# Optimization experiments

Measured on AMD Instinct MI355X. Metric: run time of the kernel, lower is better.

The kernel has to match this reference:

```python
import jax, jax.numpy as jnp
import numpy as np

T, B, I, H = 256, 32, 128, 256
CLIP = 2.0

def setup_inputs() -> dict:
    key = jax.random.key(0)
    ks = jax.random.split(key, 10)
    si, sh = 1.0 / np.sqrt(I), 1.0 / np.sqrt(H)
    return {
        "x":     jax.random.normal(ks[0], (T, B, I), jnp.float32),
        "Wx":    jax.random.normal(ks[1], (4 * H, I), jnp.float32) * si,
        "bx":    jax.random.normal(ks[2], (4 * H,), jnp.float32) * si,
        "Wh":    jax.random.normal(ks[3], (4 * H, H), jnp.float32) * sh,
        "bh":    jax.random.normal(ks[4], (4 * H,), jnp.float32) * sh,
        "w_mod": jax.random.normal(ks[5], (1, H), jnp.float32) * sh,
        "b_mod": jax.random.normal(ks[6], (1,), jnp.float32) * sh,
        "w_fan": jax.random.normal(ks[7], (H, 1), jnp.float32),
        "b_fan": jax.random.normal(ks[8], (H,), jnp.float32),
        "alpha": 1e-4 * jax.random.uniform(ks[9], (H, H), jnp.float32),
    }

def reference(x, Wx, bx, Wh, bh, w_mod, b_mod, w_fan, b_fan, alpha):
    Bn = x.shape[1]
    # precompute input projection for all timesteps: [T, B, 4H]
    xf = jnp.einsum('tbi,gi->tbg', x, Wx) + bx

    def step(state, xf_t):
        h, c, hebb = state  # h,c: [B,H]; hebb: [B,H,H]
        fioj = xf_t + h @ Wh.T + bh                     # [B,4H]
        f = jax.nn.sigmoid(fioj[:, :H])
        i = jax.nn.sigmoid(fioj[:, H:2 * H])
        o = jax.nn.sigmoid(fioj[:, 2 * H:3 * H])
        # h_pred @ (alpha * hebb) : batched vec-mat product
        plast = jnp.einsum('bh,hk,bhk->bk', h, alpha, hebb)
        j = jnp.tanh(fioj[:, 3 * H:] + plast)
        c_new = f * c + i * j
        h_new = o * jnp.tanh(c_new)
        eta = jnp.tanh(c_new @ w_mod.T + b_mod)          # [B,1]
        myeta = eta * w_fan[:, 0] + b_fan                # [B,H] (Linear(1,H) fanout)
        # delta_hebb = outer(h_pred, j); eta modulates along the j axis
        hebb_new = jnp.clip(hebb + myeta[:, None, :] * (h[:, :, None] * j[:, None, :]),
                            -CLIP, CLIP)
        return (h_new, c_new, hebb_new), h_new

    init = (jnp.zeros((Bn, H), jnp.float32),
            jnp.zeros((Bn, H), jnp.float32),
            jnp.zeros((Bn, H, H), jnp.float32))
    (h, c, hebb), hs = jax.lax.scan(step, init, xf)
    return hs, h, c, hebb
```

## Files before the change

### kernel.cpp

```cpp
#include <hip/hip_runtime.h>


#define TT 256
#define BB 32
#define II 128
#define HH 256
#define G4 1024

typedef _Float16 h2_t __attribute__((ext_vector_type(2)));
typedef unsigned long long u64;

__device__ __forceinline__ float sigm(float x) {
    return 1.0f / (1.0f + __expf(-x));
}
__device__ __forceinline__ float tanhfast(float x) {
    return 1.0f - 2.0f / (__expf(2.0f * x) + 1.0f);
}
__device__ __forceinline__ unsigned pkh(float lo, float hi) {
    h2_t v;
    v.x = (_Float16)lo;
    v.y = (_Float16)hi;
    return __builtin_bit_cast(unsigned, v);
}

__device__ __forceinline__ void bar_lds() {
    asm volatile("s_waitcnt lgkmcnt(0)\n\ts_barrier" ::: "memory");
}

#if __has_builtin(__builtin_amdgcn_fdot2)
__device__ __forceinline__ float dot2(unsigned a, unsigned b, float c) {
    return __builtin_amdgcn_fdot2(__builtin_bit_cast(h2_t, a),
                                  __builtin_bit_cast(h2_t, b), c, false);
}
#else
__device__ __forceinline__ float dot2(unsigned a, unsigned b, float c) {
    h2_t av = __builtin_bit_cast(h2_t, a), bv = __builtin_bit_cast(h2_t, b);
    return c + (float)av.x * (float)bv.x + (float)av.y * (float)bv.y;
}
#endif

__device__ __forceinline__ h2_t pkfma(h2_t a, h2_t b, h2_t c) {
#if __has_builtin(__builtin_elementwise_fma)
    return __builtin_elementwise_fma(a, b, c);
#else
    return a * b + c;
#endif
}
__device__ __forceinline__ h2_t clip2h(h2_t x) {
    const h2_t lo = {(_Float16)-2.0f, (_Float16)-2.0f};
    const h2_t hi = {(_Float16)2.0f, (_Float16)2.0f};
#if __has_builtin(__builtin_elementwise_max) && __has_builtin(__builtin_elementwise_min)
    return __builtin_elementwise_min(__builtin_elementwise_max(x, lo), hi);
#else
    h2_t r = x;
    r.x = r.x < lo.x ? lo.x : (r.x > hi.x ? hi.x : r.x);
    r.y = r.y < lo.y ? lo.y : (r.y > hi.y ? hi.y : r.y);
    return r;
#endif
}

__device__ __forceinline__ void ld3_fast(const u64* p1, const u64* p2,
                                         const u64* p3,
                                         u64& v1, u64& v2, u64& v3) {
    asm volatile(
        "global_load_dwordx2 %0, %3, off sc0\n\t"
        "global_load_dwordx2 %1, %4, off sc0\n\t"
        "global_load_dwordx2 %2, %5, off sc0\n\t"
        "s_waitcnt vmcnt(0)"
        : "=&v"(v1), "=&v"(v2), "=&v"(v3)
        : "v"(p1), "v"(p2), "v"(p3));
}

__global__ __launch_bounds__(256) void prep_wd3(const float* __restrict__ Wh,
                                                uint4* __restrict__ Wd3) {
    int idx = blockIdx.x * 256 + threadIdx.x;
    int ro = idx >> 12, rem = idx & 4095;
    int g = rem >> 2, ri = rem & 3;
    int r8 = 4 * ro + ri;
    const float4* s = (const float4*)(Wh + (size_t)g * HH + (r8 << 3));
    float4 a = s[0], b2 = s[1];
    uint4 o;
    o.x = pkh(a.x, a.y);
    o.y = pkh(a.z, a.w);
    o.z = pkh(b2.x, b2.y);
    o.w = pkh(b2.z, b2.w);
    Wd3[idx] = o;
}

__global__ __launch_bounds__(256) void prep_alq(const float* __restrict__ alpha,
                                                uint4* __restrict__ alQ) {
    int idx = blockIdx.x * 256 + threadIdx.x;
    int p4 = idx >> 8, k = idx & 255;
    unsigned r[4];
#pragma unroll
    for (int j = 0; j < 4; ++j) {
        int p = 4 * p4 + j;
        float a0 = alpha[(size_t)(2 * p) * HH + k];
        float a1 = alpha[(size_t)(2 * p + 1) * HH + k];
        r[j] = pkh(a0, a1);
    }
    uint4 o; o.x = r[0]; o.y = r[1]; o.z = r[2]; o.w = r[3];
    alQ[idx] = o;
}

__global__ __launch_bounds__(256) void xf_gemm(const float* __restrict__ x,
                                               const float* __restrict__ Wx,
                                               const float* __restrict__ bx,
                                               const float* __restrict__ bh,
                                               float* __restrict__ xf) {
    __shared__ float As[64][37];
    __shared__ float Bs[64][37];
    const int tid = threadIdx.x;
    const int tx = tid & 15, ty = tid >> 4;
    const int m0 = blockIdx.y << 6;
    const int n0 = blockIdx.x << 6;
    float c[4][4] = {};

    for (int k0 = 0; k0 < II; k0 += 32) {
#pragma unroll
        for (int hh = 0; hh < 2; ++hh) {
            int row = (tid >> 3) + (hh << 5);
            int col = (tid & 7) << 2;
            float4 va = *(const float4*)(x + (size_t)(m0 + row) * II + k0 + col);
            As[row][col] = va.x; As[row][col + 1] = va.y;
            As[row][col + 2] = va.z; As[row][col + 3] = va.w;
            float4 vb = *(const float4*)(Wx + (size_t)(n0 + row) * II + k0 + col);
            Bs[row][col] = vb.x; Bs[row][col + 1] = vb.y;
            Bs[row][col + 2] = vb.z; Bs[row][col + 3] = vb.w;
        }
        __syncthreads();
#pragma unroll
        for (int kk = 0; kk < 32; ++kk) {
            float a[4], bb[4];
#pragma unroll
            for (int u = 0; u < 4; ++u) a[u] = As[(ty << 2) + u][kk];
#pragma unroll
            for (int v = 0; v < 4; ++v) bb[v] = Bs[(tx << 2) + v][kk];
#pragma unroll
            for (int u = 0; u < 4; ++u)
#pragma unroll
                for (int v = 0; v < 4; ++v)
                    c[u][v] = fmaf(a[u], bb[v], c[u][v]);
        }
        __syncthreads();
    }
    const int n = n0 + (tx << 2);
    float4 bxv = *(const float4*)(bx + n);
    float4 bhv = *(const float4*)(bh + n);
    float4 badd = {bxv.x + bhv.x, bxv.y + bhv.y, bxv.z + bhv.z, bxv.w + bhv.w};
#pragma unroll
    for (int u = 0; u < 4; ++u) {
        int m = m0 + (ty << 2) + u;
        float4 o = {c[u][0] + badd.x, c[u][1] + badd.y,
                    c[u][2] + badd.z, c[u][3] + badd.w};
        *(float4*)(xf + (size_t)m * G4 + n) = o;
    }
}

#define HBQ_FOREACH(X) X(0) X(1) X(2) X(3) X(4) X(5) X(6) X(7)

#define HBQ_DECL(i) h2_t hp##i = {(_Float16)0.0f, (_Float16)0.0f};
#define HBQ_OUT(i) \
    hbout[(size_t)(r0g + 2 * i) * HH + k]     = (float)hp##i.x; \
    hbout[(size_t)(r0g + 2 * i + 1) * HH + k] = (float)hp##i.y;

#define HBQ_STEP(i, au, hou, hnu) { \
    h2_t al2 = __builtin_bit_cast(h2_t, au); \
    h2_t ho2 = __builtin_bit_cast(h2_t, hou); \
    h2_t hn2 = __builtin_bit_cast(h2_t, hnu); \
    hp##i = clip2h(pkfma(mj2, ho2, hp##i)); \
    h2_t hna = hn2 * al2; \
    pp = dot2(__builtin_bit_cast(unsigned, hna), \
              __builtin_bit_cast(unsigned, hp##i), pp); }

#define HBQ_CHUNK(q, AV, i0, i1, i2, i3) { \
    uint4 ho = hfO4[hb4 + (q)]; \
    uint4 hn = hfN4[hb4 + (q)]; \
    HBQ_STEP(i0, AV.x, ho.x, hn.x) \
    HBQ_STEP(i1, AV.y, ho.y, hn.y) \
    HBQ_STEP(i2, AV.z, ho.z, hn.z) \
    HBQ_STEP(i3, AV.w, ho.w, hn.w) }

#define HBV_STEP(i, hou) { \
    h2_t ho2 = __builtin_bit_cast(h2_t, hou); \
    hp##i = clip2h(pkfma(mj2, ho2, hp##i)); }
#define HBV_CHUNK(q, i0, i1, i2, i3) { \
    uint4 ho = hfO4[hb4 + (q)]; \
    HBV_STEP(i0, ho.x) HBV_STEP(i1, ho.y) \
    HBV_STEP(i2, ho.z) HBV_STEP(i3, ho.w) }

#define DOTW(W, HV) { \
    ac0 = dot2(W.x, HV.x, ac0); ac1 = dot2(W.y, HV.y, ac1); \
    ac2 = dot2(W.z, HV.z, ac2); ac3 = dot2(W.w, HV.w, ac3); }

#define PUBLISH(val) { \
    u64 pkv = ((u64)tag << 32) | (u64)__builtin_bit_cast(unsigned, val); \
    __hip_atomic_store(&myF[off], pkv, __ATOMIC_RELAXED, \
                       __HIP_MEMORY_SCOPE_WORKGROUP); \
    __hip_atomic_store(&myEx[off], pkv, __ATOMIC_RELAXED, \
                       __HIP_MEMORY_SCOPE_AGENT); }

__global__ __launch_bounds__(1024, 1) void scan_kernel(
    const float* __restrict__ xf,
    const uint4* __restrict__ Wd3,
    const uint4* __restrict__ alQ,
    const float* __restrict__ w_mod,
    const float* __restrict__ b_mod,
    const float* __restrict__ w_fan,
    const float* __restrict__ b_fan,
    u64* __restrict__ exData,
    u64* __restrict__ exFast,
    float* __restrict__ out) {
    const int bid = blockIdx.x;
    const int r   = bid >> 5;
    const int b   = bid & 31;
    const int tid = threadIdx.x;
    const int k   = tid & (HH - 1);
    const int rg  = tid >> 8;
    const int r0g = r * 64 + rg * 16;
    const int hb4 = r0g >> 3;

    __shared__ alignas(16) unsigned short hf_s[2][HH];
    __shared__ float fioj_s[G4];
    __shared__ float pp_s[4][HH];
    __shared__ float red_s[4];

    HBQ_FOREACH(HBQ_DECL)

    if (tid < HH) {
        hf_s[0][tid] = 0;
        hf_s[1][tid] = 0;
    }
    if (tid < 4) red_s[tid] = 0.0f;
    __syncthreads();

    const float bmod = b_mod[0];
    const float wf = w_fan[k], bf = b_fan[k], wm = w_mod[k];
    float creg = 0.0f, jreg = 0.0f, hnreg = 0.0f;

    const uint4* wb = Wd3 + ((size_t)(2 * r) << 12) + (tid << 2);
    uint4 w0 = wb[0], w1 = wb[1], w2 = wb[2], w3 = wb[3];
    uint4 w4 = wb[4096], w5 = wb[4097], w6 = wb[4098], w7 = wb[4099];
    uint4 aqA = alQ[(size_t)(8 * r + 2 * rg) * 256 + k];
    uint4 aqB = alQ[(size_t)(8 * r + 2 * rg + 1) * 256 + k];

    const float* xfp = xf + (size_t)b * G4 + tid;
    float xcur = (rg == r) ? xfp[0] : 0.0f;

    u64* myEx = exData + (size_t)((b * 4 + r) * 2) * 1024;
    const u64* pEx1 = exData + (size_t)((b * 4 + ((r + 1) & 3)) * 2) * 1024;
    const u64* pEx2 = exData + (size_t)((b * 4 + ((r + 2) & 3)) * 2) * 1024;
    const u64* pEx3 = exData + (size_t)((b * 4 + ((r + 3) & 3)) * 2) * 1024;
    u64* myF = exFast + (size_t)((b * 4 + r) * 2) * 1024;
    const u64* pF1 = exFast + (size_t)((b * 4 + ((r + 1) & 3)) * 2) * 1024;
    const u64* pF2 = exFast + (size_t)((b * 4 + ((r + 2) & 3)) * 2) * 1024;
    const u64* pF3 = exFast + (size_t)((b * 4 + ((r + 3) & 3)) * 2) * 1024;

    for (int t = 0; t < TT; ++t) {
        float xnext = 0.0f;
        if (rg == r && t + 1 < TT) xnext = xfp[(size_t)(t + 1) * BB * G4];

        const unsigned tag = (unsigned)(t + 1);
        const int off = (t & 1) * 1024 + tid;

        float eta = tanhfast(((red_s[0] + red_s[1]) + (red_s[2] + red_s[3])) + bmod);
        float mj = fmaf(eta, wf, bf) * jreg;
        h2_t mj2;
        mj2.x = (_Float16)mj;
        mj2.y = mj2.x;
        const uint4* hfO4 = (const uint4*)hf_s[t & 1];
        const uint4* hfN4 = (const uint4*)hf_s[(t & 1) ^ 1];
        float pp = 0.0f;
        HBQ_CHUNK(0, aqA, 0, 1, 2, 3)
        HBQ_CHUNK(1, aqB, 4, 5, 6, 7)
        pp_s[rg][k] = pp;

        float ac0 = 0.f, ac1 = 0.f, ac2 = 0.f, ac3 = 0.f;
        {
            const int hx = r << 3;
            uint4 h0 = hfN4[hx], h1 = hfN4[hx + 1];
            uint4 h2 = hfN4[hx + 2], h3 = hfN4[hx + 3];
            DOTW(w0, h0) DOTW(w1, h1) DOTW(w2, h2) DOTW(w3, h3)
            uint4 h4 = hfN4[hx + 4], h5 = hfN4[hx + 5];
            uint4 h6 = hfN4[hx + 6], h7 = hfN4[hx + 7];
            DOTW(w4, h4) DOTW(w5, h5) DOTW(w6, h6) DOTW(w7, h7)
        }
        float part = ((ac0 + ac1) + (ac2 + ac3)) + xcur;
        xcur = xnext;

        if (tid < 768) PUBLISH(part)
        bar_lds();

        if (tid >= 768) {
            int k2 = tid - 768;
            part += (pp_s[0][k2] + pp_s[1][k2]) + (pp_s[2][k2] + pp_s[3][k2]);
            PUBLISH(part)
        }

        {
            float s1 = 0.f, s2 = 0.f, s3 = 0.f;
            bool d1 = false, d2 = false, d3 = false;
            const u64* f1 = pF1 + off;
            const u64* f2 = pF2 + off;
            const u64* f3 = pF3 + off;
            int it = 0;
            do {
                u64 v1, v2, v3;
                if ((it & 3) != 3) {
                    ld3_fast(f1, f2, f3, v1, v2, v3);
                } else {
                    v1 = __hip_atomic_load(pEx1 + off, __ATOMIC_RELAXED,
                                           __HIP_MEMORY_SCOPE_AGENT);
                    v2 = __hip_atomic_load(pEx2 + off, __ATOMIC_RELAXED,
                                           __HIP_MEMORY_SCOPE_AGENT);
                    v3 = __hip_atomic_load(pEx3 + off, __ATOMIC_RELAXED,
                                           __HIP_MEMORY_SCOPE_AGENT);
                }
                ++it;
                if (!d1 && (unsigned)(v1 >> 32) == tag) {
                    s1 = __builtin_bit_cast(float, (unsigned)v1);
                    d1 = true;
                }
                if (!d2 && (unsigned)(v2 >> 32) == tag) {
                    s2 = __builtin_bit_cast(float, (unsigned)v2);
                    d2 = true;
                }
                if (!d3 && (unsigned)(v3 >> 32) == tag) {
                    s3 = __builtin_bit_cast(float, (unsigned)v3);
                    d3 = true;
                }
            } while (!(d1 && d2 && d3));
            fioj_s[tid] = part + ((s1 + s2) + s3);
        }
        bar_lds();

        jreg = tanhfast(fioj_s[3 * HH + k]);
        if (rg == 0) {
            float fg = sigm(fioj_s[k]);
            float ig = sigm(fioj_s[HH + k]);
            float og = sigm(fioj_s[2 * HH + k]);
            creg = fmaf(fg, creg, ig * jreg);
            hnreg = og * tanhfast(creg);
            _Float16 hh = (_Float16)hnreg;
            hf_s[t & 1][k] = __builtin_bit_cast(unsigned short, hh);
            if (r == 0) out[((size_t)t * BB + b) * HH + k] = hnreg;
            float e = creg * wm;
#pragma unroll
            for (int m = 32; m >= 1; m >>= 1) e += __shfl_xor(e, m, 64);
            if ((k & 63) == 0) red_s[k >> 6] = e;
        }
        bar_lds();
    }

    {
        float eta = tanhfast(((red_s[0] + red_s[1]) + (red_s[2] + red_s[3])) + bmod);
        float mj = fmaf(eta, wf, bf) * jreg;
        h2_t mj2;
        mj2.x = (_Float16)mj;
        mj2.y = mj2.x;
        const uint4* hfO4 = (const uint4*)hf_s[0];
        HBV_CHUNK(0, 0, 1, 2, 3)
        HBV_CHUNK(1, 4, 5, 6, 7)
    }

    const size_t HS = (size_t)TT * BB * HH;
    if (r == 0 && rg == 0) {
        out[HS + (size_t)b * HH + k]           = hnreg;
        out[HS + BB * HH + (size_t)b * HH + k] = creg;
    }
    float* hbout = out + HS + 2 * BB * HH + (size_t)b * HH * HH;
    HBQ_FOREACH(HBQ_OUT)
}

extern "C" void kernel_launch(void* const* d_in, const int* in_sizes, int n_in,
                              void* d_out, int out_size, void* d_ws,
                              size_t ws_size, hipStream_t stream) {
    const float* x     = (const float*)d_in[0];
    const float* Wx    = (const float*)d_in[1];
    const float* bx    = (const float*)d_in[2];
    const float* Wh    = (const float*)d_in[3];
    const float* bh    = (const float*)d_in[4];
    const float* w_mod = (const float*)d_in[5];
    const float* b_mod = (const float*)d_in[6];
    const float* w_fan = (const float*)d_in[7];
    const float* b_fan = (const float*)d_in[8];
    const float* alpha = (const float*)d_in[9];
    float* out = (float*)d_out;

    float* xf  = (float*)d_ws;
    uint4* Wd3 = (uint4*)((char*)d_ws + 33554432);
    uint4* alQ = (uint4*)((char*)d_ws + 34078720);
    u64*   exD = (u64*)((char*)d_ws + 34209792);
    u64*   exF = (u64*)((char*)d_ws + 36306944);

    hipLaunchKernelGGL(prep_wd3, dim3(128), dim3(256), 0, stream, Wh, Wd3);
    hipLaunchKernelGGL(prep_alq, dim3(32), dim3(256), 0, stream, alpha, alQ);
    hipLaunchKernelGGL(xf_gemm, dim3(16, 128), dim3(256), 0, stream,
                       x, Wx, bx, bh, xf);
    hipLaunchKernelGGL(scan_kernel, dim3(128), dim3(1024), 0, stream,
                       xf, Wd3, alQ, w_mod, b_mod, w_fan, b_fan,
                       exD, exF, out);
}
```

Before: 758.7 us.

## Interleave gate rows so each thread quad computes LSTM cell via shuffles

The recurrent weight rows are permuted so the four gates of one hidden unit land in adjacent lanes of a thread quad. Each thread applies its gate activation in place and exchanges the four values through lane shuffles, and all 1024 threads run the cell update redundantly. This removes the fioj shared-memory round trip and one block barrier per timestep, and spreads the transcendental work across all threads. In exchange it adds shuffle and select overhead, redundant cell updates, and a 16-way reduction for eta.

```diff
diff --git a/kernel.cpp b/kernel.cpp
--- a/kernel.cpp
+++ b/kernel.cpp
@@ -75,10 +75,11 @@
                                                 uint4* __restrict__ Wd3) {
     int idx = blockIdx.x * 256 + threadIdx.x;
     int ro = idx >> 12, rem = idx & 4095;
-    int g = rem >> 2, ri = rem & 3;
+    int s = rem >> 2, ri = rem & 3;
+    int g = (s & 3) * 256 + (s >> 2);
     int r8 = 4 * ro + ri;
-    const float4* s = (const float4*)(Wh + (size_t)g * HH + (r8 << 3));
-    float4 a = s[0], b2 = s[1];
+    const float4* src = (const float4*)(Wh + (size_t)g * HH + (r8 << 3));
+    float4 a = src[0], b2 = src[1];
     uint4 o;
     o.x = pkh(a.x, a.y);
     o.y = pkh(a.z, a.w);
@@ -173,9 +174,9 @@
     pp = dot2(__builtin_bit_cast(unsigned, hna), \
               __builtin_bit_cast(unsigned, hp##i), pp); }
 
-#define HBQ_CHUNK(q, AV, i0, i1, i2, i3) { \
-    uint4 ho = hfO4[hb4 + (q)]; \
-    uint4 hn = hfN4[hb4 + (q)]; \
+#define HBQ_CHUNK(cq, AV, i0, i1, i2, i3) { \
+    uint4 ho = hfO4[hb4 + (cq)]; \
+    uint4 hn = hfN4[hb4 + (cq)]; \
     HBQ_STEP(i0, AV.x, ho.x, hn.x) \
     HBQ_STEP(i1, AV.y, ho.y, hn.y) \
     HBQ_STEP(i2, AV.z, ho.z, hn.z) \
@@ -184,8 +185,8 @@
 #define HBV_STEP(i, hou) { \
     h2_t ho2 = __builtin_bit_cast(h2_t, hou); \
     hp##i = clip2h(pkfma(mj2, ho2, hp##i)); }
-#define HBV_CHUNK(q, i0, i1, i2, i3) { \
-    uint4 ho = hfO4[hb4 + (q)]; \
+#define HBV_CHUNK(cq, i0, i1, i2, i3) { \
+    uint4 ho = hfO4[hb4 + (cq)]; \
     HBV_STEP(i0, ho.x) HBV_STEP(i1, ho.y) \
     HBV_STEP(i2, ho.z) HBV_STEP(i3, ho.w) }
 
@@ -199,6 +200,14 @@
                        __HIP_MEMORY_SCOPE_WORKGROUP); \
     __hip_atomic_store(&myEx[off], pkv, __ATOMIC_RELAXED, \
                        __HIP_MEMORY_SCOPE_AGENT); }
+
+#define ETA16() ({ \
+    const float4* rp_ = (const float4*)red_s; \
+    float4 e0_ = rp_[0], e1_ = rp_[1], e2_ = rp_[2], e3_ = rp_[3]; \
+    (((e0_.x + e0_.y) + (e0_.z + e0_.w)) + \
+     ((e1_.x + e1_.y) + (e1_.z + e1_.w))) + \
+    (((e2_.x + e2_.y) + (e2_.z + e2_.w)) + \
+     ((e3_.x + e3_.y) + (e3_.z + e3_.w))); })
 
 __global__ __launch_bounds__(1024, 1) void scan_kernel(
     const float* __restrict__ xf,
@@ -215,28 +224,35 @@
     const int r   = bid >> 5;
     const int b   = bid & 31;
     const int tid = threadIdx.x;
+    const int wv  = tid >> 6;
+    const int l   = tid & 63;
+    const int q   = tid & 3;
+    const int kc  = tid >> 2;
+    const int g   = (q << 8) + kc;
     const int k   = tid & (HH - 1);
     const int rg  = tid >> 8;
     const int r0g = r * 64 + rg * 16;
     const int hb4 = r0g >> 3;
 
     __shared__ alignas(16) unsigned short hf_s[2][HH];
-    __shared__ float fioj_s[G4];
     __shared__ float pp_s[4][HH];
-    __shared__ float red_s[4];
+    __shared__ float js_s[HH];
+    __shared__ alignas(16) float red_s[16];
 
     HBQ_FOREACH(HBQ_DECL)
 
     if (tid < HH) {
         hf_s[0][tid] = 0;
         hf_s[1][tid] = 0;
-    }
-    if (tid < 4) red_s[tid] = 0.0f;
+        js_s[tid] = 0.0f;
+    }
+    if (tid < 16) red_s[tid] = 0.0f;
     __syncthreads();
 
     const float bmod = b_mod[0];
-    const float wf = w_fan[k], bf = b_fan[k], wm = w_mod[k];
-    float creg = 0.0f, jreg = 0.0f, hnreg = 0.0f;
+    const float wf = w_fan[k], bf = b_fan[k];
+    const float wmq = 0.25f * w_mod[kc];
+    float creg = 0.0f, hreg = 0.0f;
 
     const uint4* wb = Wd3 + ((size_t)(2 * r) << 12) + (tid << 2);
     uint4 w0 = wb[0], w1 = wb[1], w2 = wb[2], w3 = wb[3];
@@ -244,8 +260,8 @@
     uint4 aqA = alQ[(size_t)(8 * r + 2 * rg) * 256 + k];
     uint4 aqB = alQ[(size_t)(8 * r + 2 * rg + 1) * 256 + k];
 
-    const float* xfp = xf + (size_t)b * G4 + tid;
-    float xcur = (rg == r) ? xfp[0] : 0.0f;
+    const float* xfp = xf + (size_t)b * G4 + g;
+    float xcur = (q == r) ? xfp[0] : 0.0f;
 
     u64* myEx = exData + (size_t)((b * 4 + r) * 2) * 1024;
     const u64* pEx1 = exData + (size_t)((b * 4 + ((r + 1) & 3)) * 2) * 1024;
@@ -258,13 +274,14 @@
 
     for (int t = 0; t < TT; ++t) {
         float xnext = 0.0f;
-        if (rg == r && t + 1 < TT) xnext = xfp[(size_t)(t + 1) * BB * G4];
+        if (q == r && t + 1 < TT) xnext = xfp[(size_t)(t + 1) * BB * G4];
 
         const unsigned tag = (unsigned)(t + 1);
         const int off = (t & 1) * 1024 + tid;
 
-        float eta = tanhfast(((red_s[0] + red_s[1]) + (red_s[2] + red_s[3])) + bmod);
-        float mj = fmaf(eta, wf, bf) * jreg;
+        float eta = tanhfast(ETA16() + bmod);
+        float jls = js_s[k];
+        float mj = fmaf(eta, wf, bf) * jls;
         h2_t mj2;
         mj2.x = (_Float16)mj;
         mj2.y = mj2.x;
@@ -288,15 +305,15 @@
         float part = ((ac0 + ac1) + (ac2 + ac3)) + xcur;
         xcur = xnext;
 
-        if (tid < 768) PUBLISH(part)
+        if (q != 3) PUBLISH(part)
         bar_lds();
 
-        if (tid >= 768) {
-            int k2 = tid - 768;
-            part += (pp_s[0][k2] + pp_s[1][k2]) + (pp_s[2][k2] + pp_s[3][k2]);
+        if (q == 3) {
+            part += (pp_s[0][kc] + pp_s[1][kc]) + (pp_s[2][kc] + pp_s[3][kc]);
             PUBLISH(part)
         }
 
+        float tot;
         {
             float s1 = 0.f, s2 = 0.f, s3 = 0.f;
             bool d1 = false, d2 = false, d3 = false;
@@ -330,31 +347,45 @@
                     d3 = true;
                 }
             } while (!(d1 && d2 && d3));
-            fioj_s[tid] = part + ((s1 + s2) + s3);
-        }
+            tot = part + ((s1 + s2) + s3);
+        }
+
+        float scale = (q == 3) ? 2.0f : 1.0f;
+        float sg = 1.0f / (1.0f + __expf(-scale * tot));
+        float act = fmaf(sg, scale, (q == 3) ? -1.0f : 0.0f);
+
+        float x1v = __shfl_xor(act, 1, 64);
+        float x2v = __shfl_xor(act, 2, 64);
+        float x3v = __shfl_xor(x1v, 2, 64);
+        bool sA = (q & 1) != 0, sB = (q & 2) != 0;
+        float b0 = sA ? x1v : act;
+        float b1 = sA ? act : x1v;
+        float b2v = sA ? x3v : x2v;
+        float b3v = sA ? x2v : x3v;
+        float fg = sB ? b2v : b0;
+        float og = sB ? b0 : b2v;
+        float ig = sB ? b3v : b1;
+        float jg = sB ? b1 : b3v;
+
+        creg = fmaf(fg, creg, ig * jg);
+        hreg = og * tanhfast(creg);
+        if (q == 0) {
+            _Float16 hh = (_Float16)hreg;
+            hf_s[t & 1][kc] = __builtin_bit_cast(unsigned short, hh);
+            js_s[kc] = jg;
+            if (r == 0) out[((size_t)t * BB + b) * HH + kc] = hreg;
+        }
+        float e = creg * wmq;
+#pragma unroll
+        for (int m = 32; m >= 1; m >>= 1) e += __shfl_xor(e, m, 64);
+        if (l == 0) red_s[wv] = e;
+
         bar_lds();
-
-        jreg = tanhfast(fioj_s[3 * HH + k]);
-        if (rg == 0) {
-            float fg = sigm(fioj_s[k]);
-            float ig = sigm(fioj_s[HH + k]);
-            float og = sigm(fioj_s[2 * HH + k]);
-            creg = fmaf(fg, creg, ig * jreg);
-            hnreg = og * tanhfast(creg);
-            _Float16 hh = (_Float16)hnreg;
-            hf_s[t & 1][k] = __builtin_bit_cast(unsigned short, hh);
-            if (r == 0) out[((size_t)t * BB + b) * HH + k] = hnreg;
-            float e = creg * wm;
-#pragma unroll
-            for (int m = 32; m >= 1; m >>= 1) e += __shfl_xor(e, m, 64);
-            if ((k & 63) == 0) red_s[k >> 6] = e;
-        }
-        bar_lds();
     }
 
     {
-        float eta = tanhfast(((red_s[0] + red_s[1]) + (red_s[2] + red_s[3])) + bmod);
-        float mj = fmaf(eta, wf, bf) * jreg;
+        float eta = tanhfast(ETA16() + bmod);
+        float mj = fmaf(eta, wf, bf) * js_s[k];
         h2_t mj2;
         mj2.x = (_Float16)mj;
         mj2.y = mj2.x;
@@ -364,9 +395,9 @@
     }
 
     const size_t HS = (size_t)TT * BB * HH;
-    if (r == 0 && rg == 0) {
-        out[HS + (size_t)b * HH + k]           = hnreg;
-        out[HS + BB * HH + (size_t)b * HH + k] = creg;
+    if (r == 0 && q == 0) {
+        out[HS + (size_t)b * HH + kc]           = hreg;
+        out[HS + BB * HH + (size_t)b * HH + kc] = creg;
     }
     float* hbout = out + HS + 2 * BB * HH + (size_t)b * HH * HH;
     HBQ_FOREACH(HBQ_OUT)
```

After: 894.1 us. 17.9% more time.
